# Kernel tuning notes

Measured on AMD Instinct MI355X. Metric: run time of the kernel, lower is better.

Reference implementation:

```python
import jax, jax.numpy as jnp
import numpy as np

MULTI_SCALE = [1, 3, 7, 9]
H = 8          # attention heads
EPS = 1e-8     # torch F.cosine_similarity eps


def _roi_avg_pool(feats_bct, rois, n_bins):
    """Temporal ROI adaptive average pooling (assumed behavior of `avr(i)`).
    feats_bct: [B, C, T]; rois: [N, 3] int (batch_idx, start, end) -> [N, C, n_bins].
    Bin b covers [s + floor(b*L/n), s + ceil((b+1)*L/n)) like adaptive_avg_pool1d.
    """
    T = feats_bct.shape[2]
    bidx, s, e = rois[:, 0], rois[:, 1], rois[:, 2]
    L = (e - s)[:, None, None]                               # [N,1,1]
    b = jnp.arange(n_bins, dtype=rois.dtype)[None, :, None]  # [1,nb,1]
    t = jnp.arange(T, dtype=rois.dtype)[None, None, :]       # [1,1,T]
    bs = s[:, None, None] + (b * L) // n_bins                # floor
    be = s[:, None, None] - (-(b + 1) * L) // n_bins         # ceil
    mask = ((t >= bs) & (t < be)).astype(feats_bct.dtype)    # [N,nb,T]
    mask = mask / jnp.clip(mask.sum(-1, keepdims=True), 1.0)
    roi_feats = feats_bct[bidx]                              # [N,C,T]
    return jnp.einsum('nit,nct->nci', mask, roi_feats)


def setup_inputs() -> dict:
    key = jax.random.key(0)
    ks = jax.random.split(key, 16)
    B, D, T, N = 4, 1024, 2048, 128
    hec = len(MULTI_SCALE)
    Cg = D // hec  # 256 channels per scale group
    inp = {
        'input_vectors': jax.random.normal(ks[0], (B, D, T), jnp.float32),
        'clstoken_scales': jax.random.normal(ks[1], (B, D), jnp.float32),
    }
    # rois: (batch_idx, start, end) with end > start
    bidx = jax.random.randint(ks[2], (N,), 0, B, jnp.int32)
    s = jax.random.randint(ks[3], (N,), 0, T // 2, jnp.int32)
    length = jax.random.randint(ks[4], (N,), 16, T // 2, jnp.int32)
    inp['rois'] = jnp.stack([bidx, s, jnp.minimum(s + length, T)], axis=1)
    sc = 1.0 / np.sqrt(D)
    inp['Wq'] = jax.random.normal(ks[5], (D, D), jnp.float32) * sc
    inp['bq'] = jnp.zeros((D,), jnp.float32)
    inp['Wk'] = jax.random.normal(ks[6], (D, D), jnp.float32) * sc
    inp['bk'] = jnp.zeros((D,), jnp.float32)
    inp['Wv'] = jax.random.normal(ks[7], (D, D), jnp.float32) * sc
    inp['bv'] = jnp.zeros((D,), jnp.float32)
    for j, nb in enumerate(MULTI_SCALE):
        csc = 1.0 / np.sqrt(Cg * nb)
        inp[f'conv_w{nb}'] = jax.random.normal(ks[8 + j], (Cg, Cg, nb), jnp.float32) * csc
        inp[f'conv_b{nb}'] = jnp.zeros((Cg,), jnp.float32)
    return inp


def reference(input_vectors, clstoken_scales, rois, Wq, bq, Wk, bk, Wv, bv,
              conv_w1, conv_b1, conv_w3, conv_b3, conv_w7, conv_b7, conv_w9, conv_b9):
    B, D, T = input_vectors.shape
    dk = D // H
    hec = len(MULTI_SCALE)
    x = input_vectors.transpose(0, 2, 1)                     # [B,T,D]
    # projections (torch Linear: y = x W^T + b)
    q = clstoken_scales @ Wq.T + bq                          # [B,D]
    k = (x @ Wk.T + bk).reshape(B, T, H, dk).transpose(0, 2, 1, 3)  # [B,H,T,dk]
    v = (x @ Wv.T + bv).reshape(B, T, H, dk).transpose(0, 2, 1, 3)  # [B,H,T,dk]
    qh = q.reshape(B, H, 1, dk)                              # [B,H,1,dk]
    # cosine-similarity pseudo-attention (no repeat blow-up: broadcast instead)
    dot = jnp.einsum('bhqd,bhtd->bht', qh, k)                # [B,H,T]
    nq = jnp.linalg.norm(qh, axis=-1)                        # [B,H,1]
    nk = jnp.linalg.norm(k, axis=-1)                         # [B,H,T]
    cos = dot / jnp.maximum(nq * nk, EPS)
    # eval mode: mask is all-ones, dropout identity
    p_attn = jnp.exp(jnp.abs(cos))                           # [B,H,T]
    val = p_attn[..., None] * v                              # [B,H,T,dk]
    # permute(0,1,3,2).view(B, hec, -1, T): group 2 heads per scale
    val = val.transpose(0, 1, 3, 2).reshape(B, hec, (H // hec) * dk, T)
    conv_ws = [conv_w1, conv_w3, conv_w7, conv_w9]
    conv_bs = [conv_b1, conv_b3, conv_b7, conv_b9]
    outs = []
    for j, nb in enumerate(MULTI_SCALE):
        pooled = _roi_avg_pool(val[:, j], rois, nb)          # [N, D//hec, nb]
        # Conv3d kernel (nb,1,1) stride (nb,1,1) on [N,C,nb,1,1] == full contraction
        outs.append(jnp.einsum('nci,oci->no', pooled, conv_ws[j]) + conv_bs[j])
    return jnp.concatenate(outs, axis=1)                     # [N_roi, D]
```

## Files before the change

kernel.cpp:

```cpp
#include <hip/hip_runtime.h>
#include <hip/hip_bf16.h>
#include <math.h>

#define BB   4
#define DD   1024
#define TT   2048
#define NH   8
#define DKH  128
#define NROI 128

typedef __attribute__((ext_vector_type(8))) __bf16 bf16x8;
typedef __attribute__((ext_vector_type(4))) float  f32x4;

#define OFF_Q    0
#define OFF_KV   131072
#define OFF_POOL (131072 + 8388608)
#define POOL_FLOATS 655360
#define WS_F32_TOTAL (OFF_POOL + POOL_FLOATS)

__device__ __forceinline__ float bfu2f(unsigned short u) {
    return __uint_as_float(((unsigned int)u) << 16);
}

__global__ __launch_bounds__(256) void qproj_kernel(
    const float* __restrict__ cls, const float* __restrict__ Wq,
    const float* __restrict__ bq, float* __restrict__ q)
{
    const int blk  = blockIdx.x;
    const int b    = blk >> 8;
    const int dg   = blk & 255;
    const int warp = threadIdx.x >> 6;
    const int lane = threadIdx.x & 63;
    const int d    = dg * 4 + warp;
    const float* crow = cls + (size_t)b * DD;
    const float* wrow = Wq + (size_t)d * DD;
    float acc = 0.f;
    for (int i = lane; i < DD; i += 64) acc += crow[i] * wrow[i];
    #pragma unroll
    for (int off = 32; off; off >>= 1) acc += __shfl_down(acc, off);
    if (lane == 0) q[(size_t)b * DD + d] = acc + bq[d];
}

__global__ __launch_bounds__(256) void convert_pair(
    const float* __restrict__ A, const float* __restrict__ B,
    __hip_bfloat16* __restrict__ Ab, __hip_bfloat16* __restrict__ Bb)
{
    const int i = blockIdx.x * 256 + threadIdx.x;
    float4 a = reinterpret_cast<const float4*>(A)[i];
    float4 b = reinterpret_cast<const float4*>(B)[i];
    union P4 { __hip_bfloat16 h[4]; ushort4 u; } pa, pb;
    pa.h[0] = __float2bfloat16(a.x); pa.h[1] = __float2bfloat16(a.y);
    pa.h[2] = __float2bfloat16(a.z); pa.h[3] = __float2bfloat16(a.w);
    pb.h[0] = __float2bfloat16(b.x); pb.h[1] = __float2bfloat16(b.y);
    pb.h[2] = __float2bfloat16(b.z); pb.h[3] = __float2bfloat16(b.w);
    reinterpret_cast<ushort4*>(Ab)[i] = pa.u;
    reinterpret_cast<ushort4*>(Bb)[i] = pb.u;
}

__global__ __launch_bounds__(256) void transpose_convert(
    const float* __restrict__ X, __hip_bfloat16* __restrict__ Xt)
{
    __shared__ float tile[64][65];
    const int t0 = blockIdx.x * 64, d0 = blockIdx.y * 64, b = blockIdx.z;
    const int tid = threadIdx.x;
    const float* src = X + ((size_t)(b * DD + d0)) * TT + t0;
    const int f4c = tid & 15;
    const int r0  = tid >> 4;
    #pragma unroll
    for (int i = 0; i < 4; ++i) {
        const int r = r0 + 16 * i;
        const float4 v = *reinterpret_cast<const float4*>(&src[(size_t)r * TT + f4c * 4]);
        tile[r][f4c * 4 + 0] = v.x;
        tile[r][f4c * 4 + 1] = v.y;
        tile[r][f4c * 4 + 2] = v.z;
        tile[r][f4c * 4 + 3] = v.w;
    }
    __syncthreads();
    const int lane = tid & 63, w = tid >> 6;
    const int dq = (lane & 15) * 4;
    const int th = lane >> 4;
    __hip_bfloat16* dst = Xt + ((size_t)(b * TT + t0)) * DD + d0;
    #pragma unroll
    for (int i = 0; i < 4; ++i) {
        const int t = w * 4 + th + i * 16;
        union { __hip_bfloat16 h[4]; ushort4 u; } P;
        P.h[0] = __float2bfloat16(tile[dq + 0][t]);
        P.h[1] = __float2bfloat16(tile[dq + 1][t]);
        P.h[2] = __float2bfloat16(tile[dq + 2][t]);
        P.h[3] = __float2bfloat16(tile[dq + 3][t]);
        *reinterpret_cast<ushort4*>(&dst[(size_t)t * DD + dq]) = P.u;
    }
}

__device__ __forceinline__ void glds16(const __hip_bfloat16* g, __hip_bfloat16* l)
{
    __builtin_amdgcn_global_load_lds(
        (const __attribute__((address_space(1))) void*)g,
        (__attribute__((address_space(3))) void*)l, 16, 0, 0);
}

__global__ __launch_bounds__(512) void fused_kv(
    const __hip_bfloat16* __restrict__ Wkb,
    const __hip_bfloat16* __restrict__ Wvb,
    const __hip_bfloat16* __restrict__ Xt,
    const float* __restrict__ bk, const float* __restrict__ bv,
    const float* __restrict__ q,
    __hip_bfloat16* __restrict__ val)
{
    const int t0 = blockIdx.x * 128;
    const int m0 = blockIdx.y * 128;
    const int b  = blockIdx.z;

    __shared__ __hip_bfloat16 AsK[2][128 * 32];
    __shared__ __hip_bfloat16 AsV[2][128 * 32];
    __shared__ __hip_bfloat16 Bs[2][128 * 32];
    __shared__ float qs[128];
    __shared__ float rdot[2][128];
    __shared__ float rsq[2][128];
    __shared__ float p_lds[128];

    const int tid  = threadIdx.x;
    const int lane = tid & 63;
    const int w    = tid >> 6;
    const int wr   = w >> 2;
    const int wc   = w & 3;

    if (tid < 128) qs[tid] = q[(size_t)b * DD + m0 + tid];

    const int st_row = tid >> 2;
    const int st_g   = (tid & 3) ^ ((st_row >> 1) & 3);

    const __hip_bfloat16* WkS = Wkb + (size_t)(m0 + st_row) * DD + st_g * 8;
    const __hip_bfloat16* WvS = Wvb + (size_t)(m0 + st_row) * DD + st_g * 8;
    const __hip_bfloat16* XS  = Xt + ((size_t)(b * TT + t0 + st_row)) * DD + st_g * 8;
    const int ldsoff = (w * 16) * 32;

    f32x4 ak[4][2], av[4][2];
    #pragma unroll
    for (int i = 0; i < 4; ++i)
        #pragma unroll
        for (int j = 0; j < 2; ++j) {
            ak[i][j] = (f32x4){0.f, 0.f, 0.f, 0.f};
            av[i][j] = (f32x4){0.f, 0.f, 0.f, 0.f};
        }

    auto STAGE = [&](int buf, int k0) {
        glds16(WkS + k0, AsK[buf] + ldsoff);
        glds16(WvS + k0, AsV[buf] + ldsoff);
        glds16(XS  + k0, Bs[buf]  + ldsoff);
    };

    auto COMPUTE = [&](int buf) {
        const int g = lane >> 4;
        bf16x8 bfx[2], afk[4], afv[4];
        #pragma unroll
        for (int fn = 0; fn < 2; ++fn) {
            const int r = wc * 32 + fn * 16 + (lane & 15);
            const int s = g ^ ((r >> 1) & 3);
            bfx[fn] = *reinterpret_cast<const bf16x8*>(&Bs[buf][r * 32 + s * 8]);
        }
        #pragma unroll
        for (int fm = 0; fm < 4; ++fm) {
            const int r = wr * 64 + fm * 16 + (lane & 15);
            const int s = g ^ ((r >> 1) & 3);
            afk[fm] = *reinterpret_cast<const bf16x8*>(&AsK[buf][r * 32 + s * 8]);
            afv[fm] = *reinterpret_cast<const bf16x8*>(&AsV[buf][r * 32 + s * 8]);
        }
        #pragma unroll
        for (int fm = 0; fm < 4; ++fm)
            #pragma unroll
            for (int fn = 0; fn < 2; ++fn)
                ak[fm][fn] = __builtin_amdgcn_mfma_f32_16x16x32_bf16(
                    afk[fm], bfx[fn], ak[fm][fn], 0, 0, 0);
        #pragma unroll
        for (int fm = 0; fm < 4; ++fm)
            #pragma unroll
            for (int fn = 0; fn < 2; ++fn)
                av[fm][fn] = __builtin_amdgcn_mfma_f32_16x16x32_bf16(
                    afv[fm], bfx[fn], av[fm][fn], 0, 0, 0);
    };

    STAGE(0, 0);
    STAGE(1, 32);
    asm volatile("s_waitcnt lgkmcnt(0)" ::: "memory");
    int cur = 0;
    #pragma unroll 2
    for (int i = 0; i < 30; ++i) {
        asm volatile("s_waitcnt vmcnt(3)" ::: "memory");
        __builtin_amdgcn_s_barrier();
        COMPUTE(cur);
        __builtin_amdgcn_s_barrier();
        STAGE(cur, (i + 2) * 32);
        cur ^= 1;
    }
    asm volatile("s_waitcnt vmcnt(3)" ::: "memory");
    __builtin_amdgcn_s_barrier();
    COMPUTE(cur);
    cur ^= 1;
    asm volatile("s_waitcnt vmcnt(0)" ::: "memory");
    __builtin_amdgcn_s_barrier();
    COMPUTE(cur);

    const int lg = lane >> 4;
    #pragma unroll
    for (int fn = 0; fn < 2; ++fn) {
        float dp = 0.f, sp = 0.f;
        #pragma unroll
        for (int fm = 0; fm < 4; ++fm) {
            const int mb = wr * 64 + fm * 16 + lg * 4;
            #pragma unroll
            for (int r = 0; r < 4; ++r) {
                const float kv = ak[fm][fn][r] + bk[m0 + mb + r];
                dp += kv * qs[mb + r];
                sp += kv * kv;
            }
        }
        dp += __shfl_xor(dp, 16); sp += __shfl_xor(sp, 16);
        dp += __shfl_xor(dp, 32); sp += __shfl_xor(sp, 32);
        if (lane < 16) {
            rdot[wr][wc * 32 + fn * 16 + lane] = dp;
            rsq[wr][wc * 32 + fn * 16 + lane]  = sp;
        }
    }
    __syncthreads();
    if (tid < 128) {
        const float dd = rdot[0][tid] + rdot[1][tid];
        const float ss = rsq[0][tid] + rsq[1][tid];
        float qn2 = 0.f;
        for (int j = 0; j < 128; ++j) qn2 += qs[j] * qs[j];
        const float c = dd / fmaxf(sqrtf(qn2) * sqrtf(ss), 1e-8f);
        p_lds[tid] = expf(fabsf(c));
    }
    __syncthreads();

    float pv[2];
    #pragma unroll
    for (int fn = 0; fn < 2; ++fn)
        pv[fn] = p_lds[wc * 32 + fn * 16 + (lane & 15)];

    const int tbase = t0 + wc * 32 + (lane & 15);
    #pragma unroll
    for (int fm = 0; fm < 4; ++fm) {
        const int m = m0 + wr * 64 + fm * 16 + lg * 4;
        const float4 b4 = *reinterpret_cast<const float4*>(&bv[m]);
        #pragma unroll
        for (int fn = 0; fn < 2; ++fn) {
            const int t = tbase + fn * 16;
            const f32x4 a = av[fm][fn];
            const float pf = pv[fn];
            union { __hip_bfloat16 h[4]; ushort4 u; } P;
            P.h[0] = __float2bfloat16((a[0] + b4.x) * pf);
            P.h[1] = __float2bfloat16((a[1] + b4.y) * pf);
            P.h[2] = __float2bfloat16((a[2] + b4.z) * pf);
            P.h[3] = __float2bfloat16((a[3] + b4.w) * pf);
            *reinterpret_cast<ushort4*>(&val[((size_t)(b * TT + t)) * DD + m]) = P.u;
        }
    }
}

#define POOL_WAVES 16
__global__ __launch_bounds__(1024) void pool_kernel(
    const __hip_bfloat16* __restrict__ val, const int* __restrict__ rois,
    float* __restrict__ pooled)
{
    const int n    = blockIdx.x;
    const int sc   = blockIdx.y;
    const int tid  = threadIdx.x;
    const int lane = tid & 63;
    const int w    = tid >> 6;

    const int nbt[4]  = {1, 3, 7, 9};
    const int offt[4] = {0, 32768, 131072, 360448};
    const int nb  = nbt[sc];
    const int off = offt[sc];

    __shared__ float lacc[9][256];
    for (int i = tid; i < nb * 256; i += 1024)
        ((float*)lacc)[i] = 0.f;

    const int bidx = rois[n * 3 + 0];
    const int s    = rois[n * 3 + 1];
    const int e    = rois[n * 3 + 2];
    const int L    = e - s;
    __syncthreads();

    const int ts = s + (w * L) / POOL_WAVES;
    const int te = s + ((w + 1) * L) / POOL_WAVES;

    const int cq = lane * 4;
    const __hip_bfloat16* vb = val + (size_t)bidx * TT * DD + sc * 256 + cq;

    if (te > ts) {
        int bin = ((ts - s) * nb) / L;
        int nbs = s + ((bin + 1) * L) / nb;
        int cbe = s + ((bin + 1) * L + nb - 1) / nb;

        if (bin > 0 && ts < s + (bin * L + nb - 1) / nb) {
            const ushort4 u = *reinterpret_cast<const ushort4*>(&vb[(size_t)ts * DD]);
            atomicAdd(&lacc[bin - 1][cq + 0], bfu2f(u.x));
            atomicAdd(&lacc[bin - 1][cq + 1], bfu2f(u.y));
            atomicAdd(&lacc[bin - 1][cq + 2], bfu2f(u.z));
            atomicAdd(&lacc[bin - 1][cq + 3], bfu2f(u.w));
        }

        float a0 = 0.f, a1 = 0.f, a2 = 0.f, a3 = 0.f;
        int t = ts;
        while (true) {
            const int seg = min(te, nbs);
            for (; t + 8 <= seg; t += 8) {
                ushort4 u[8];
                #pragma unroll
                for (int jj = 0; jj < 8; ++jj)
                    u[jj] = *reinterpret_cast<const ushort4*>(&vb[(size_t)(t + jj) * DD]);
                #pragma unroll
                for (int jj = 0; jj < 8; ++jj) {
                    a0 += bfu2f(u[jj].x); a1 += bfu2f(u[jj].y);
                    a2 += bfu2f(u[jj].z); a3 += bfu2f(u[jj].w);
                }
            }
            for (; t < seg; ++t) {
                const ushort4 u = *reinterpret_cast<const ushort4*>(&vb[(size_t)t * DD]);
                a0 += bfu2f(u.x); a1 += bfu2f(u.y);
                a2 += bfu2f(u.z); a3 += bfu2f(u.w);
            }
            if (t >= te) break;
            const ushort4 u = *reinterpret_cast<const ushort4*>(&vb[(size_t)t * DD]);
            const float v0 = bfu2f(u.x), v1 = bfu2f(u.y),
                        v2 = bfu2f(u.z), v3 = bfu2f(u.w);
            if (t < cbe) { a0 += v0; a1 += v1; a2 += v2; a3 += v3; }
            atomicAdd(&lacc[bin][cq + 0], a0);
            atomicAdd(&lacc[bin][cq + 1], a1);
            atomicAdd(&lacc[bin][cq + 2], a2);
            atomicAdd(&lacc[bin][cq + 3], a3);
            a0 = v0; a1 = v1; a2 = v2; a3 = v3;
            ++bin; ++t;
            nbs = s + ((bin + 1) * L) / nb;
            cbe = s + ((bin + 1) * L + nb - 1) / nb;
        }
        atomicAdd(&lacc[bin][cq + 0], a0);
        atomicAdd(&lacc[bin][cq + 1], a1);
        atomicAdd(&lacc[bin][cq + 2], a2);
        atomicAdd(&lacc[bin][cq + 3], a3);
    }
    __syncthreads();

    float* po = pooled + off + (size_t)n * 256 * nb;
    for (int i = tid; i < nb * 256; i += 1024) {
        const int bin = i >> 8, ch = i & 255;
        const int bs  = s + (bin * L) / nb;
        const int be  = s + ((bin + 1) * L + nb - 1) / nb;
        po[(size_t)ch * nb + bin] = lacc[bin][ch] / (float)max(be - bs, 1);
    }
}

__global__ __launch_bounds__(256) void out_gemm(
    const float* __restrict__ pooled,
    const float* __restrict__ w1, const float* __restrict__ b1,
    const float* __restrict__ w3, const float* __restrict__ b3,
    const float* __restrict__ w7, const float* __restrict__ b7,
    const float* __restrict__ w9, const float* __restrict__ b9,
    float* __restrict__ out)
{
    const int z = blockIdx.z;
    int sc, kc;
    if      (z == 0)  { sc = 0; kc = 0; }
    else if (z < 4)   { sc = 1; kc = z - 1; }
    else if (z < 11)  { sc = 2; kc = z - 4; }
    else              { sc = 3; kc = z - 11; }

    int nb, off; const float* W; const float* bias;
    switch (sc) {
        case 0:  nb = 1; off = 0;      W = w1; bias = b1; break;
        case 1:  nb = 3; off = 32768;  W = w3; bias = b3; break;
        case 2:  nb = 7; off = 131072; W = w7; bias = b7; break;
        default: nb = 9; off = 360448; W = w9; bias = b9; break;
    }
    const int Kj = 256 * nb;
    const float* P = pooled + off;

    const int o0 = blockIdx.x * 32;
    const int n0 = blockIdx.y * 32;
    const int kbase = kc * 256;

    __shared__ float Ps[32][33];
    __shared__ float Ws[32][33];

    const int tid = threadIdx.x;
    const int tx = tid & 15, ty = tid >> 4;
    float acc[2][2] = {};

    for (int k0 = kbase; k0 < kbase + 256; k0 += 32) {
        #pragma unroll
        for (int i = 0; i < 4; ++i) {
            const int li = tid + i * 256;
            const int r = li >> 5, k = li & 31;
            Ps[r][k] = P[(size_t)(n0 + r) * Kj + k0 + k];
            Ws[r][k] = W[(size_t)(o0 + r) * Kj + k0 + k];
        }
        __syncthreads();
        #pragma unroll
        for (int k = 0; k < 32; ++k) {
            const float p0 = Ps[ty][k],  p1 = Ps[ty + 16][k];
            const float w0 = Ws[tx][k],  w1v = Ws[tx + 16][k];
            acc[0][0] = fmaf(p0, w0,  acc[0][0]);
            acc[0][1] = fmaf(p0, w1v, acc[0][1]);
            acc[1][0] = fmaf(p1, w0,  acc[1][0]);
            acc[1][1] = fmaf(p1, w1v, acc[1][1]);
        }
        __syncthreads();
    }
    #pragma unroll
    for (int i = 0; i < 2; ++i) {
        const int n = n0 + ty + 16 * i;
        #pragma unroll
        for (int jj = 0; jj < 2; ++jj) {
            const int o = o0 + tx + 16 * jj;
            const float add = (kc == 0) ? bias[o] : 0.f;
            atomicAdd(&out[(size_t)n * DD + sc * 256 + o], acc[i][jj] + add);
        }
    }
}

extern "C" void kernel_launch(void* const* d_in, const int* in_sizes, int n_in,
                              void* d_out, int out_size, void* d_ws, size_t ws_size,
                              hipStream_t stream)
{
    const float* inp  = (const float*)d_in[0];
    const float* cls  = (const float*)d_in[1];
    const int*   rois = (const int*)  d_in[2];
    const float* Wq   = (const float*)d_in[3];
    const float* bq   = (const float*)d_in[4];
    const float* Wk   = (const float*)d_in[5];
    const float* bk   = (const float*)d_in[6];
    const float* Wv   = (const float*)d_in[7];
    const float* bv   = (const float*)d_in[8];
    const float* cw1  = (const float*)d_in[9];  const float* cb1 = (const float*)d_in[10];
    const float* cw3  = (const float*)d_in[11]; const float* cb3 = (const float*)d_in[12];
    const float* cw7  = (const float*)d_in[13]; const float* cb7 = (const float*)d_in[14];
    const float* cw9  = (const float*)d_in[15]; const float* cb9 = (const float*)d_in[16];

    float* out = (float*)d_out;
    float* ws  = (float*)d_ws;
    float* q      = ws + OFF_Q;
    __hip_bfloat16* val = (__hip_bfloat16*)(ws + OFF_KV);
    float* pooled = ws + OFF_POOL;
    __hip_bfloat16* bfb = (__hip_bfloat16*)(ws + WS_F32_TOTAL);
    __hip_bfloat16* Wkb = bfb;
    __hip_bfloat16* Wvb = bfb + 1048576;
    __hip_bfloat16* Xt  = bfb + 2097152;

    convert_pair<<<dim3(1024), 256, 0, stream>>>(Wk, Wv, Wkb, Wvb);
    transpose_convert<<<dim3(TT / 64, DD / 64, BB), 256, 0, stream>>>(inp, Xt);
    qproj_kernel<<<dim3(BB * 256), 256, 0, stream>>>(cls, Wq, bq, q);
    fused_kv<<<dim3(TT / 128, DD / 128, BB), 512, 0, stream>>>(
        Wkb, Wvb, Xt, bk, bv, q, val);
    pool_kernel<<<dim3(NROI, 4), 1024, 0, stream>>>(val, rois, pooled);
    hipMemsetAsync(out, 0, (size_t)out_size * sizeof(float), stream);
    out_gemm<<<dim3(8, 4, 20), 256, 0, stream>>>(pooled, cw1, cb1, cw3, cb3,
                                                 cw7, cb7, cw9, cb9, out);
}
```

Baseline: 108.8 us.

## Precompute 8-step block sums of val and pool ROI bins from them

Adds a pass that sums every 8 consecutive time steps of the bf16 value tensor into an fp32 block-sum buffer. The pool kernel then runs one block per (ROI, bin), adding block sums for the aligned interior and reading raw rows only for the unaligned head and tail. This replaces the old per-scale streaming over every time step with shared-memory atomics, cutting the rows read per bin roughly eightfold. In exchange it adds an extra kernel and a 16 MB fp32 write and read, and it changes the fp32 summation order.

```diff
diff --git a/kernel.cpp b/kernel.cpp
--- a/kernel.cpp
+++ b/kernel.cpp
@@ -14,6 +14,7 @@
 
 #define OFF_Q    0
 #define OFF_KV   131072
+#define OFF_BS   (131072 + 4194304)
 #define OFF_POOL (131072 + 8388608)
 #define POOL_FLOATS 655360
 #define WS_F32_TOTAL (OFF_POOL + POOL_FLOATS)
@@ -258,99 +259,101 @@
     }
 }
 
-#define POOL_WAVES 16
-__global__ __launch_bounds__(1024) void pool_kernel(
-    const __hip_bfloat16* __restrict__ val, const int* __restrict__ rois,
-    float* __restrict__ pooled)
-{
-    const int n    = blockIdx.x;
-    const int sc   = blockIdx.y;
-    const int tid  = threadIdx.x;
-    const int lane = tid & 63;
-    const int w    = tid >> 6;
+__global__ __launch_bounds__(1024) void bs_build(
+    const __hip_bfloat16* __restrict__ val, float* __restrict__ BS)
+{
+    const int b  = blockIdx.y;
+    const int g  = blockIdx.x * 4 + (threadIdx.x >> 8);
+    const int c4 = (threadIdx.x & 255) * 4;
+    const __hip_bfloat16* vb = val + ((size_t)b * TT + g * 8) * DD + c4;
+    float a0 = 0.f, a1 = 0.f, a2 = 0.f, a3 = 0.f;
+    #pragma unroll
+    for (int j = 0; j < 8; ++j) {
+        const ushort4 u = *reinterpret_cast<const ushort4*>(&vb[(size_t)j * DD]);
+        a0 += bfu2f(u.x); a1 += bfu2f(u.y);
+        a2 += bfu2f(u.z); a3 += bfu2f(u.w);
+    }
+    float4 r; r.x = a0; r.y = a1; r.z = a2; r.w = a3;
+    *reinterpret_cast<float4*>(&BS[((size_t)b * 256 + g) * DD + c4]) = r;
+}
+
+__global__ __launch_bounds__(256) void pool_kernel(
+    const __hip_bfloat16* __restrict__ val, const float* __restrict__ BS,
+    const int* __restrict__ rois, float* __restrict__ pooled)
+{
+    const int n = blockIdx.x;
+    const int z = blockIdx.y;
+    int sc, bin;
+    if      (z == 0)  { sc = 0; bin = 0; }
+    else if (z < 4)   { sc = 1; bin = z - 1; }
+    else if (z < 11)  { sc = 2; bin = z - 4; }
+    else              { sc = 3; bin = z - 11; }
 
     const int nbt[4]  = {1, 3, 7, 9};
     const int offt[4] = {0, 32768, 131072, 360448};
     const int nb  = nbt[sc];
     const int off = offt[sc];
 
-    __shared__ float lacc[9][256];
-    for (int i = tid; i < nb * 256; i += 1024)
-        ((float*)lacc)[i] = 0.f;
-
     const int bidx = rois[n * 3 + 0];
     const int s    = rois[n * 3 + 1];
     const int e    = rois[n * 3 + 2];
     const int L    = e - s;
-    __syncthreads();
-
-    const int ts = s + (w * L) / POOL_WAVES;
-    const int te = s + ((w + 1) * L) / POOL_WAVES;
-
-    const int cq = lane * 4;
-    const __hip_bfloat16* vb = val + (size_t)bidx * TT * DD + sc * 256 + cq;
-
-    if (te > ts) {
-        int bin = ((ts - s) * nb) / L;
-        int nbs = s + ((bin + 1) * L) / nb;
-        int cbe = s + ((bin + 1) * L + nb - 1) / nb;
-
-        if (bin > 0 && ts < s + (bin * L + nb - 1) / nb) {
-            const ushort4 u = *reinterpret_cast<const ushort4*>(&vb[(size_t)ts * DD]);
-            atomicAdd(&lacc[bin - 1][cq + 0], bfu2f(u.x));
-            atomicAdd(&lacc[bin - 1][cq + 1], bfu2f(u.y));
-            atomicAdd(&lacc[bin - 1][cq + 2], bfu2f(u.z));
-            atomicAdd(&lacc[bin - 1][cq + 3], bfu2f(u.w));
-        }
-
-        float a0 = 0.f, a1 = 0.f, a2 = 0.f, a3 = 0.f;
-        int t = ts;
-        while (true) {
-            const int seg = min(te, nbs);
-            for (; t + 8 <= seg; t += 8) {
-                ushort4 u[8];
-                #pragma unroll
-                for (int jj = 0; jj < 8; ++jj)
-                    u[jj] = *reinterpret_cast<const ushort4*>(&vb[(size_t)(t + jj) * DD]);
-                #pragma unroll
-                for (int jj = 0; jj < 8; ++jj) {
-                    a0 += bfu2f(u[jj].x); a1 += bfu2f(u[jj].y);
-                    a2 += bfu2f(u[jj].z); a3 += bfu2f(u[jj].w);
-                }
-            }
-            for (; t < seg; ++t) {
+
+    const int bs  = s + (bin * L) / nb;
+    const int be  = s + ((bin + 1) * L + nb - 1) / nb;
+    const int cnt = be - bs;
+
+    const int tid     = threadIdx.x;
+    const int quarter = tid >> 6;
+    const int lane    = tid & 63;
+    const int c4      = lane * 4;
+
+    const __hip_bfloat16* vb = val + (size_t)bidx * TT * DD + sc * 256 + c4;
+    const float* bsrc = BS + (size_t)bidx * 256 * DD + sc * 256 + c4;
+
+    float a0 = 0.f, a1 = 0.f, a2 = 0.f, a3 = 0.f;
+    const int g_lo = (bs + 7) >> 3;
+    const int g_hi = be >> 3;
+
+    if (g_lo >= g_hi) {
+        for (int t = bs + quarter; t < be; t += 4) {
+            const ushort4 u = *reinterpret_cast<const ushort4*>(&vb[(size_t)t * DD]);
+            a0 += bfu2f(u.x); a1 += bfu2f(u.y);
+            a2 += bfu2f(u.z); a3 += bfu2f(u.w);
+        }
+    } else {
+        const int ngrp  = g_hi - g_lo;
+        const int nhead = g_lo * 8 - bs;
+        const int ntail = be - g_hi * 8;
+        const int nitems = ngrp + nhead + ntail;
+        for (int i = quarter; i < nitems; i += 4) {
+            if (i < ngrp) {
+                const float4 v = *reinterpret_cast<const float4*>(
+                    &bsrc[(size_t)(g_lo + i) * DD]);
+                a0 += v.x; a1 += v.y; a2 += v.z; a3 += v.w;
+            } else if (i < ngrp + nhead) {
+                const int t = bs + (i - ngrp);
+                const ushort4 u = *reinterpret_cast<const ushort4*>(&vb[(size_t)t * DD]);
+                a0 += bfu2f(u.x); a1 += bfu2f(u.y);
+                a2 += bfu2f(u.z); a3 += bfu2f(u.w);
+            } else {
+                const int t = g_hi * 8 + (i - ngrp - nhead);
                 const ushort4 u = *reinterpret_cast<const ushort4*>(&vb[(size_t)t * DD]);
                 a0 += bfu2f(u.x); a1 += bfu2f(u.y);
                 a2 += bfu2f(u.z); a3 += bfu2f(u.w);
             }
-            if (t >= te) break;
-            const ushort4 u = *reinterpret_cast<const ushort4*>(&vb[(size_t)t * DD]);
-            const float v0 = bfu2f(u.x), v1 = bfu2f(u.y),
-                        v2 = bfu2f(u.z), v3 = bfu2f(u.w);
-            if (t < cbe) { a0 += v0; a1 += v1; a2 += v2; a3 += v3; }
-            atomicAdd(&lacc[bin][cq + 0], a0);
-            atomicAdd(&lacc[bin][cq + 1], a1);
-            atomicAdd(&lacc[bin][cq + 2], a2);
-            atomicAdd(&lacc[bin][cq + 3], a3);
-            a0 = v0; a1 = v1; a2 = v2; a3 = v3;
-            ++bin; ++t;
-            nbs = s + ((bin + 1) * L) / nb;
-            cbe = s + ((bin + 1) * L + nb - 1) / nb;
-        }
-        atomicAdd(&lacc[bin][cq + 0], a0);
-        atomicAdd(&lacc[bin][cq + 1], a1);
-        atomicAdd(&lacc[bin][cq + 2], a2);
-        atomicAdd(&lacc[bin][cq + 3], a3);
-    }
+        }
+    }
+
+    __shared__ float lacc[4][256];
+    float4 r; r.x = a0; r.y = a1; r.z = a2; r.w = a3;
+    *reinterpret_cast<float4*>(&lacc[quarter][c4]) = r;
     __syncthreads();
 
-    float* po = pooled + off + (size_t)n * 256 * nb;
-    for (int i = tid; i < nb * 256; i += 1024) {
-        const int bin = i >> 8, ch = i & 255;
-        const int bs  = s + (bin * L) / nb;
-        const int be  = s + ((bin + 1) * L + nb - 1) / nb;
-        po[(size_t)ch * nb + bin] = lacc[bin][ch] / (float)max(be - bs, 1);
-    }
+    const int ch = tid;
+    const float v = (lacc[0][ch] + lacc[1][ch] + lacc[2][ch] + lacc[3][ch])
+                    / (float)cnt;
+    pooled[off + ((size_t)n * 256 + ch) * nb + bin] = v;
 }
 
 __global__ __launch_bounds__(256) void out_gemm(
@@ -443,6 +446,7 @@
     float* ws  = (float*)d_ws;
     float* q      = ws + OFF_Q;
     __hip_bfloat16* val = (__hip_bfloat16*)(ws + OFF_KV);
+    float* BS     = ws + OFF_BS;
     float* pooled = ws + OFF_POOL;
     __hip_bfloat16* bfb = (__hip_bfloat16*)(ws + WS_F32_TOTAL);
     __hip_bfloat16* Wkb = bfb;
@@ -454,7 +458,8 @@
     qproj_kernel<<<dim3(BB * 256), 256, 0, stream>>>(cls, Wq, bq, q);
     fused_kv<<<dim3(TT / 128, DD / 128, BB), 512, 0, stream>>>(
         Wkb, Wvb, Xt, bk, bv, q, val);
-    pool_kernel<<<dim3(NROI, 4), 1024, 0, stream>>>(val, rois, pooled);
+    bs_build<<<dim3(64, BB), 1024, 0, stream>>>(val, BS);
+    pool_kernel<<<dim3(NROI, 20), 256, 0, stream>>>(val, BS, rois, pooled);
     hipMemsetAsync(out, 0, (size_t)out_size * sizeof(float), stream);
     out_gemm<<<dim3(8, 4, 20), 256, 0, stream>>>(pooled, cw1, cb1, cw3, cb3,
                                                  cw7, cb7, cw9, cb9, out);
```

Result: faster. 99.68 us (-8.4%).
